# Optimization experiments

Hardware: AMD Instinct MI355X
Metric: run time of the kernel (lower is better)

Reference implementation:

```python
import jax, jax.numpy as jnp
import numpy as np

B, S, IN, OUT = 4, 4096, 4096, 4096

def setup_inputs() -> dict:
    key = jax.random.key(0)
    k1, k2, k3 = jax.random.split(key, 3)
    x = jax.random.normal(k1, (B, S, IN), dtype=jnp.float32)
    # packed ternary weight: (sign+1) in {0,1,2}, stored as small int
    packed_w = jax.random.randint(k2, (OUT, IN), 0, 3, dtype=jnp.int32)
    # alpha = mean(|W|) surrogate; act_scale = max|x|/127 surrogate
    alpha = jnp.float32(0.02)
    act_scale = jnp.float32(4.0 / 127.0)
    bias = jax.random.normal(k3, (OUT,), dtype=jnp.float32)
    return {"x": x, "packed_w": packed_w, "alpha": alpha, "act_scale": act_scale, "bias": bias}

def reference(x, packed_w, alpha, act_scale, bias):
    # Activation fake-quant (int8 symmetric): round(x/scale), clamp, dequant.
    # torch uses act_scale.item() -> scale is a constant w.r.t. autodiff.
    scale = jax.lax.stop_gradient(jnp.maximum(act_scale, 1e-5))
    x_int = jnp.clip(jnp.round(x / scale), -127.0, 127.0)
    x_dq = jnp.nan_to_num(x_int * scale, nan=0.0, posinf=10000.0, neginf=-10000.0)
    # Ternary weight dequant: (packed - 1) * alpha, values in {-a, 0, +a}
    w = (packed_w.astype(jnp.float32) - 1.0) * alpha  # [OUT, IN]
    # F.linear: x @ W^T + b
    return jnp.einsum('bsi,oi->bso', x_dq, w) + bias
```

## Files before the change

kernel.cpp:

```cpp
#include <hip/hip_runtime.h>
#include <hip/hip_bf16.h>

typedef int v4i __attribute__((ext_vector_type(4)));

#define M_DIM 16384
#define N_DIM 4096
#define K_DIM 4096
#define BM 256
#define BN 256
#define BKB 128
#define NT (K_DIM / BKB)

__global__ void quant_x_kernel(const float4* __restrict__ x, int* __restrict__ q,
                               const float* __restrict__ act_scale, int n4) {
  const float s = fmaxf(act_scale[0], 1e-5f);
  int i = blockIdx.x * blockDim.x + threadIdx.x;
  const int stride = gridDim.x * blockDim.x;
  for (; i < n4; i += stride) {
    float4 v = x[i];
    int b0 = (int)fminf(fmaxf(rintf(v.x / s), -127.f), 127.f);
    int b1 = (int)fminf(fmaxf(rintf(v.y / s), -127.f), 127.f);
    int b2 = (int)fminf(fmaxf(rintf(v.z / s), -127.f), 127.f);
    int b3 = (int)fminf(fmaxf(rintf(v.w / s), -127.f), 127.f);
    q[i] = (b0 & 0xff) | ((b1 & 0xff) << 8) | ((b2 & 0xff) << 16) | ((b3 & 0xff) << 24);
  }
}

__global__ void pack_w_kernel(const int4* __restrict__ w, int* __restrict__ q, int n4) {
  int i = blockIdx.x * blockDim.x + threadIdx.x;
  const int stride = gridDim.x * blockDim.x;
  for (; i < n4; i += stride) {
    int4 v = w[i];
    q[i] = ((v.x - 1) & 0xff) | (((v.y - 1) & 0xff) << 8) |
           (((v.z - 1) & 0xff) << 16) | (((v.w - 1) & 0xff) << 24);
  }
}

__global__ __launch_bounds__(512, 2) void bitlinear_gemm(
    const signed char* __restrict__ A,
    const signed char* __restrict__ B,
    const float* __restrict__ bias,
    const float* __restrict__ alpha_p,
    const float* __restrict__ act_scale_p,
    float* __restrict__ out) {
  __shared__ __align__(16) signed char As0[BM * BKB];
  __shared__ __align__(16) signed char As1[BM * BKB];
  __shared__ __align__(16) signed char Bs0[BN * BKB];
  __shared__ __align__(16) signed char Bs1[BN * BKB];

  const int t = threadIdx.x;
  const int lane = t & 63, wid = t >> 6;
  const int wm = wid >> 2, wn = wid & 3;
  const int l15 = lane & 15, l4 = lane >> 4;

  const int nwg = (M_DIM / BM) * (N_DIM / BN);
  const int wg = (blockIdx.x & 7) * (nwg >> 3) + (blockIdx.x >> 3);
  const int bm = wg / (N_DIM / BN);
  const int bn = wg % (N_DIM / BN);

  const int dmaSeg = wid * 4096;
  const signed char* aD = A + ((size_t)(bm * BM + 32 * wid + (lane >> 3))) * K_DIM
                            + (((lane & 7) ^ (lane >> 3)) * 16);
  const signed char* bD = B + ((size_t)(bn * BN + 32 * wid + (lane >> 3))) * K_DIM
                            + (((lane & 7) ^ (lane >> 3)) * 16);

#define DMA4(SRCBASE, DSTARR, KOFF) \
  { _Pragma("unroll") for (int i = 0; i < 4; ++i) \
      __builtin_amdgcn_global_load_lds( \
        (const __attribute__((address_space(1))) void*)((SRCBASE) + (size_t)(8 * i) * K_DIM + (KOFF)), \
        (__attribute__((address_space(3))) void*)(&(DSTARR)[dmaSeg + i * 1024]), \
        16, 0, 0); }

  const int l7 = l15 & 7;
  const int soK0 = ((0 + l4) ^ l7) * 16;
  const int soK1 = ((4 + l4) ^ l7) * 16;
  const int aRd = (wm * 128 + l15) * BKB;
  const int bRd = (wn * 64 + l15) * BKB;

  v4i acc[8][4] = {};
  v4i bF[4][2], aF[2][2];

#define LOAD_B(BS) \
  { _Pragma("unroll") for (int nc = 0; nc < 4; ++nc) { \
      bF[nc][0] = *(const v4i*)&(BS)[bRd + nc * 2048 + soK0]; \
      bF[nc][1] = *(const v4i*)&(BS)[bRd + nc * 2048 + soK1]; } }

#define LOAD_A(AS, q) \
  aF[0][0] = *(const v4i*)&(AS)[aRd + (2*(q)) * 2048 + soK0]; \
  aF[0][1] = *(const v4i*)&(AS)[aRd + (2*(q)) * 2048 + soK1]; \
  aF[1][0] = *(const v4i*)&(AS)[aRd + (2*(q)+1) * 2048 + soK0]; \
  aF[1][1] = *(const v4i*)&(AS)[aRd + (2*(q)+1) * 2048 + soK1];

#define MFMA_Q(q) \
  { _Pragma("unroll") for (int nc = 0; nc < 4; ++nc) { \
      acc[2*(q)][nc]   = __builtin_amdgcn_mfma_i32_16x16x64_i8(aF[0][0], bF[nc][0], acc[2*(q)][nc], 0, 0, 0); \
      acc[2*(q)][nc]   = __builtin_amdgcn_mfma_i32_16x16x64_i8(aF[0][1], bF[nc][1], acc[2*(q)][nc], 0, 0, 0); \
      acc[2*(q)+1][nc] = __builtin_amdgcn_mfma_i32_16x16x64_i8(aF[1][0], bF[nc][0], acc[2*(q)+1][nc], 0, 0, 0); \
      acc[2*(q)+1][nc] = __builtin_amdgcn_mfma_i32_16x16x64_i8(aF[1][1], bF[nc][1], acc[2*(q)+1][nc], 0, 0, 0); } }

#define BAR __builtin_amdgcn_s_barrier()

#define TILE_BODY(ASR, BSR, ASW, BSW, KNEXT) do { \
    DMA4(bD, BSW, KNEXT); \
    DMA4(aD, ASW, KNEXT); \
    LOAD_B(BSR); LOAD_A(ASR, 0); \
    __builtin_amdgcn_s_setprio(1); MFMA_Q(0); __builtin_amdgcn_s_setprio(0); \
    LOAD_A(ASR, 1); \
    __builtin_amdgcn_s_setprio(1); MFMA_Q(1); __builtin_amdgcn_s_setprio(0); \
    LOAD_A(ASR, 2); \
    __builtin_amdgcn_s_setprio(1); MFMA_Q(2); __builtin_amdgcn_s_setprio(0); \
    LOAD_A(ASR, 3); \
    __builtin_amdgcn_s_setprio(1); MFMA_Q(3); __builtin_amdgcn_s_setprio(0); \
    asm volatile("s_waitcnt vmcnt(0) lgkmcnt(0)" ::: "memory"); \
    BAR; \
  } while (0)

  DMA4(bD, Bs0, 0);
  DMA4(aD, As0, 0);
  asm volatile("s_waitcnt vmcnt(0)" ::: "memory");
  BAR;
  __builtin_amdgcn_sched_barrier(0);

  for (int it = 0; it < NT / 2 - 1; ++it) {
    TILE_BODY(As0, Bs0, As1, Bs1, (2 * it + 1) * BKB);
    TILE_BODY(As1, Bs1, As0, Bs0, (2 * it + 2) * BKB);
  }
  TILE_BODY(As0, Bs0, As1, Bs1, 31 * BKB);
  TILE_BODY(As1, Bs1, As0, Bs0, 31 * BKB);

  const float sA_ = fmaxf(act_scale_p[0], 1e-5f) * alpha_p[0];
  const int gn0 = bn * BN + wn * 64 + l15;
  const int gm0 = bm * BM + wm * 128 + l4 * 4;
#pragma unroll
  for (int nc = 0; nc < 4; ++nc) {
    const float bv = bias[gn0 + nc * 16];
#pragma unroll
    for (int mr = 0; mr < 8; ++mr) {
#pragma unroll
      for (int r = 0; r < 4; ++r) {
        const int gm = gm0 + mr * 16 + r;
        out[(size_t)gm * N_DIM + gn0 + nc * 16] = (float)acc[mr][nc][r] * sA_ + bv;
      }
    }
  }
}

extern "C" void kernel_launch(void* const* d_in, const int* in_sizes, int n_in,
                              void* d_out, int out_size, void* d_ws, size_t ws_size,
                              hipStream_t stream) {
  const float* x      = (const float*)d_in[0];
  const int*   pw     = (const int*)d_in[1];
  const float* alpha  = (const float*)d_in[2];
  const float* act_sc = (const float*)d_in[3];
  const float* bias   = (const float*)d_in[4];
  float* out = (float*)d_out;

  signed char* x8 = (signed char*)d_ws;
  signed char* w8 = (signed char*)d_ws + (size_t)M_DIM * K_DIM;

  quant_x_kernel<<<2048, 256, 0, stream>>>((const float4*)x, (int*)x8, act_sc, M_DIM * K_DIM / 4);
  pack_w_kernel<<<2048, 256, 0, stream>>>((const int4*)pw, (int*)w8, N_DIM * K_DIM / 4);

  dim3 grid((M_DIM / BM) * (N_DIM / BN));
  bitlinear_gemm<<<grid, 512, 0, stream>>>(x8, w8, bias, alpha, act_sc, out);
}
```

Measured before the change: 402.8 us.

## Merge prep kernels and interleave DMA with barrier-separated MFMA phases

The activation-quantisation and weight-packing kernels are merged into one launch that splits its blocks between the two jobs, and the quantiser now multiplies by a precomputed reciprocal instead of dividing. The GEMM tile body is reordered so the first LDS fragment reads are issued before the global-to-LDS DMAs. The B and A DMAs are split across different compute phases, and workgroup barriers are placed around each MFMA quarter to keep waves in lockstep. This aims to cut launch overhead and divides and to spread memory traffic across the tile, at the cost of extra barrier stalls. Multiplying by the reciprocal can round differently from true division for a few values, which may change some quantised values.

```diff
diff --git a/kernel.cpp b/kernel.cpp
--- a/kernel.cpp
+++ b/kernel.cpp
@@ -11,28 +11,33 @@
 #define BKB 128
 #define NT (K_DIM / BKB)
 
-__global__ void quant_x_kernel(const float4* __restrict__ x, int* __restrict__ q,
-                               const float* __restrict__ act_scale, int n4) {
-  const float s = fmaxf(act_scale[0], 1e-5f);
-  int i = blockIdx.x * blockDim.x + threadIdx.x;
-  const int stride = gridDim.x * blockDim.x;
-  for (; i < n4; i += stride) {
-    float4 v = x[i];
-    int b0 = (int)fminf(fmaxf(rintf(v.x / s), -127.f), 127.f);
-    int b1 = (int)fminf(fmaxf(rintf(v.y / s), -127.f), 127.f);
-    int b2 = (int)fminf(fmaxf(rintf(v.z / s), -127.f), 127.f);
-    int b3 = (int)fminf(fmaxf(rintf(v.w / s), -127.f), 127.f);
-    q[i] = (b0 & 0xff) | ((b1 & 0xff) << 8) | ((b2 & 0xff) << 16) | ((b3 & 0xff) << 24);
-  }
-}
+#define QBLK 2048
+#define PBLK 512
 
-__global__ void pack_w_kernel(const int4* __restrict__ w, int* __restrict__ q, int n4) {
-  int i = blockIdx.x * blockDim.x + threadIdx.x;
-  const int stride = gridDim.x * blockDim.x;
-  for (; i < n4; i += stride) {
-    int4 v = w[i];
-    q[i] = ((v.x - 1) & 0xff) | (((v.y - 1) & 0xff) << 8) |
-           (((v.z - 1) & 0xff) << 16) | (((v.w - 1) & 0xff) << 24);
+__global__ void prep_kernel(const float4* __restrict__ x, int* __restrict__ qx, int n4x,
+                            const int4* __restrict__ w, int* __restrict__ qw, int n4w,
+                            const float* __restrict__ act_scale) {
+  if (blockIdx.x < QBLK) {
+    const float s = fmaxf(act_scale[0], 1e-5f);
+    const float inv_s = 1.0f / s;
+    int i = blockIdx.x * blockDim.x + threadIdx.x;
+    const int stride = QBLK * blockDim.x;
+    for (; i < n4x; i += stride) {
+      float4 v = x[i];
+      int b0 = (int)fminf(fmaxf(rintf(v.x * inv_s), -127.f), 127.f);
+      int b1 = (int)fminf(fmaxf(rintf(v.y * inv_s), -127.f), 127.f);
+      int b2 = (int)fminf(fmaxf(rintf(v.z * inv_s), -127.f), 127.f);
+      int b3 = (int)fminf(fmaxf(rintf(v.w * inv_s), -127.f), 127.f);
+      qx[i] = (b0 & 0xff) | ((b1 & 0xff) << 8) | ((b2 & 0xff) << 16) | ((b3 & 0xff) << 24);
+    }
+  } else {
+    int i = (blockIdx.x - QBLK) * blockDim.x + threadIdx.x;
+    const int stride = PBLK * blockDim.x;
+    for (; i < n4w; i += stride) {
+      int4 v = w[i];
+      qw[i] = ((v.x - 1) & 0xff) | (((v.y - 1) & 0xff) << 8) |
+              (((v.z - 1) & 0xff) << 16) | (((v.w - 1) & 0xff) << 24);
+    }
   }
 }
 
@@ -99,19 +104,28 @@
       acc[2*(q)+1][nc] = __builtin_amdgcn_mfma_i32_16x16x64_i8(aF[1][1], bF[nc][1], acc[2*(q)+1][nc], 0, 0, 0); } }
 
 #define BAR __builtin_amdgcn_s_barrier()
+#define PRIO1 __builtin_amdgcn_s_setprio(1)
+#define PRIO0 __builtin_amdgcn_s_setprio(0)
 
 #define TILE_BODY(ASR, BSR, ASW, BSW, KNEXT) do { \
+    LOAD_B(BSR); LOAD_A(ASR, 0); \
     DMA4(bD, BSW, KNEXT); \
+    BAR; \
+    PRIO1; MFMA_Q(0); PRIO0; \
+    BAR; \
+    LOAD_A(ASR, 1); \
     DMA4(aD, ASW, KNEXT); \
-    LOAD_B(BSR); LOAD_A(ASR, 0); \
-    __builtin_amdgcn_s_setprio(1); MFMA_Q(0); __builtin_amdgcn_s_setprio(0); \
-    LOAD_A(ASR, 1); \
-    __builtin_amdgcn_s_setprio(1); MFMA_Q(1); __builtin_amdgcn_s_setprio(0); \
+    BAR; \
+    PRIO1; MFMA_Q(1); PRIO0; \
+    BAR; \
     LOAD_A(ASR, 2); \
-    __builtin_amdgcn_s_setprio(1); MFMA_Q(2); __builtin_amdgcn_s_setprio(0); \
+    BAR; \
+    PRIO1; MFMA_Q(2); PRIO0; \
+    BAR; \
     LOAD_A(ASR, 3); \
-    __builtin_amdgcn_s_setprio(1); MFMA_Q(3); __builtin_amdgcn_s_setprio(0); \
-    asm volatile("s_waitcnt vmcnt(0) lgkmcnt(0)" ::: "memory"); \
+    BAR; \
+    PRIO1; MFMA_Q(3); PRIO0; \
+    asm volatile("s_waitcnt vmcnt(0)" ::: "memory"); \
     BAR; \
   } while (0)
 
@@ -158,8 +172,9 @@
   signed char* x8 = (signed char*)d_ws;
   signed char* w8 = (signed char*)d_ws + (size_t)M_DIM * K_DIM;
 
-  quant_x_kernel<<<2048, 256, 0, stream>>>((const float4*)x, (int*)x8, act_sc, M_DIM * K_DIM / 4);
-  pack_w_kernel<<<2048, 256, 0, stream>>>((const int4*)pw, (int*)w8, N_DIM * K_DIM / 4);
+  prep_kernel<<<QBLK + PBLK, 256, 0, stream>>>(
+      (const float4*)x, (int*)x8, M_DIM * K_DIM / 4,
+      (const int4*)pw, (int*)w8, N_DIM * K_DIM / 4, act_sc);
 
   dim3 grid((M_DIM / BM) * (N_DIM / BN));
   bitlinear_gemm<<<grid, 512, 0, stream>>>(x8, w8, bias, alpha, act_sc, out);
```

After: 399.8 us. No clear change (-0.8%).
